# Performance work log

Measured on AMD Instinct MI355X. Metric: run time of the kernel, lower is better.

Reference implementation:

```python
import jax, jax.numpy as jnp
import numpy as np

D_MODEL = 1024
N_HEADS = 16
HEAD_DIM = D_MODEL // N_HEADS
D_FF = 4096
B, T = 2, 2048
LN_EPS = 1e-5


def setup_inputs() -> dict:
    key = jax.random.key(0)
    ks = jax.random.split(key, 12)
    s = 0.02
    return {
        "x": jax.random.normal(ks[0], (B, T, D_MODEL), jnp.float32),
        "ln1_g": jnp.ones((D_MODEL,), jnp.float32),
        "ln1_b": jnp.zeros((D_MODEL,), jnp.float32),
        "w_qkv": jax.random.normal(ks[1], (D_MODEL, 3 * D_MODEL), jnp.float32) * s,
        "b_qkv": jnp.zeros((3 * D_MODEL,), jnp.float32),
        "w_out": jax.random.normal(ks[2], (D_MODEL, D_MODEL), jnp.float32) * s,
        "b_out": jnp.zeros((D_MODEL,), jnp.float32),
        "ln2_g": jnp.ones((D_MODEL,), jnp.float32),
        "ln2_b": jnp.zeros((D_MODEL,), jnp.float32),
        "w_ff1": jax.random.normal(ks[3], (D_MODEL, D_FF), jnp.float32) * s,
        "b_ff1": jnp.zeros((D_FF,), jnp.float32),
        "w_ff2": jax.random.normal(ks[4], (D_FF, D_MODEL), jnp.float32) * s,
        "b_ff2": jnp.zeros((D_MODEL,), jnp.float32),
    }


def _layernorm(x, g, b):
    mu = jnp.mean(x, axis=-1, keepdims=True)
    var = jnp.mean(jnp.square(x - mu), axis=-1, keepdims=True)
    return (x - mu) * jax.lax.rsqrt(var + LN_EPS) * g + b


def _attention(h, w_qkv, b_qkv, w_out, b_out):
    Bx, Tx, C = h.shape
    qkv = h @ w_qkv + b_qkv  # [B,T,3C]
    q, k, v = jnp.split(qkv, 3, axis=-1)
    # [B,H,T,Dh]
    q = q.reshape(Bx, Tx, N_HEADS, HEAD_DIM).transpose(0, 2, 1, 3)
    k = k.reshape(Bx, Tx, N_HEADS, HEAD_DIM).transpose(0, 2, 1, 3)
    v = v.reshape(Bx, Tx, N_HEADS, HEAD_DIM).transpose(0, 2, 1, 3)
    scale = 1.0 / np.sqrt(HEAD_DIM).astype(np.float32)
    scores = jnp.einsum("bhqd,bhkd->bhqk", q, k) * scale
    causal = jnp.tril(jnp.ones((Tx, Tx), bool))
    scores = jnp.where(causal[None, None], scores, -jnp.inf)
    attn = jax.nn.softmax(scores, axis=-1)
    out = jnp.einsum("bhqk,bhkd->bhqd", attn, v)
    out = out.transpose(0, 2, 1, 3).reshape(Bx, Tx, C)
    return out @ w_out + b_out


def reference(x, ln1_g, ln1_b, w_qkv, b_qkv, w_out, b_out,
              ln2_g, ln2_b, w_ff1, b_ff1, w_ff2, b_ff2):
    h = _layernorm(x, ln1_g, ln1_b)
    x = x + _attention(h, w_qkv, b_qkv, w_out, b_out)
    h2 = _layernorm(x, ln2_g, ln2_b)
    ff = jax.nn.relu(h2 @ w_ff1 + b_ff1) @ w_ff2 + b_ff2
    return x + ff
```

## Files before the change

### kernel.cpp

```cpp
#include <hip/hip_runtime.h>


typedef unsigned short u16;
typedef __attribute__((ext_vector_type(8))) short     bf16x8;
typedef __attribute__((ext_vector_type(4))) float     f32x4;
typedef __attribute__((ext_vector_type(8))) unsigned short u16x8;
typedef __attribute__((ext_vector_type(4))) unsigned short u16x4;

__device__ __forceinline__ u16 f2bf(float f) {
    unsigned u = __builtin_bit_cast(unsigned, f);
    unsigned r = (u + 0x7fffu + ((u >> 16) & 1u)) >> 16;
    return (u16)r;
}
__device__ __forceinline__ float bf2f(u16 h) {
    unsigned u = ((unsigned)h) << 16;
    return __builtin_bit_cast(float, u);
}
__device__ __forceinline__ f32x4 mfma16(bf16x8 a, bf16x8 b, f32x4 c) {
    return __builtin_amdgcn_mfma_f32_16x16x32_bf16(a, b, c, 0, 0, 0);
}
__device__ __forceinline__ void gl_lds16(const u16* g, u16* l) {
    __builtin_amdgcn_global_load_lds((const __attribute__((address_space(1))) void*)g,
                                     (__attribute__((address_space(3))) void*)l, 16, 0, 0);
}

__global__ __launch_bounds__(256) void wconv_kernel(const float* __restrict__ in, u16* __restrict__ out,
                                                    int R, int C) {
    __shared__ float t[32][33];
    const int tx = threadIdx.x, ty = threadIdx.y;
    const int c0 = blockIdx.x * 32, r0 = blockIdx.y * 32;
#pragma unroll
    for (int i = 0; i < 4; ++i)
        t[ty + 8 * i][tx] = in[(size_t)(r0 + ty + 8 * i) * C + c0 + tx];
    __syncthreads();
#pragma unroll
    for (int i = 0; i < 4; ++i)
        out[(size_t)(c0 + ty + 8 * i) * R + r0 + tx] = f2bf(t[tx][ty + 8 * i]);
}

__global__ __launch_bounds__(256) void ln_kernel(const float* __restrict__ x, const float* __restrict__ g,
                                                 const float* __restrict__ b, u16* __restrict__ out) {
    const int row = blockIdx.x, tid = threadIdx.x;
    const float4 v = ((const float4*)(x + (size_t)row * 1024))[tid];
    float s = v.x + v.y + v.z + v.w;
    float q = v.x * v.x + v.y * v.y + v.z * v.z + v.w * v.w;
#pragma unroll
    for (int o = 32; o; o >>= 1) { s += __shfl_xor(s, o); q += __shfl_xor(q, o); }
    __shared__ float red[8];
    if ((tid & 63) == 0) { red[(tid >> 6) * 2] = s; red[(tid >> 6) * 2 + 1] = q; }
    __syncthreads();
    s = red[0] + red[2] + red[4] + red[6];
    q = red[1] + red[3] + red[5] + red[7];
    const float mu = s * (1.0f / 1024.0f);
    const float var = q * (1.0f / 1024.0f) - mu * mu;
    const float rs = rsqrtf(var + 1e-5f);
    const float4 gv = ((const float4*)g)[tid];
    const float4 bv = ((const float4*)b)[tid];
    u16x4 o;
    o[0] = f2bf((v.x - mu) * rs * gv.x + bv.x);
    o[1] = f2bf((v.y - mu) * rs * gv.y + bv.y);
    o[2] = f2bf((v.z - mu) * rs * gv.z + bv.z);
    o[3] = f2bf((v.w - mu) * rs * gv.w + bv.w);
    ((u16x4*)(out + (size_t)row * 1024))[tid] = o;
}

template <int MODE, int BN>
__global__ __launch_bounds__(256) void gemm_kernel(const u16* __restrict__ A, const u16* __restrict__ Bt,
                                                   const float* __restrict__ bias, const float* __restrict__ resid,
                                                   void* __restrict__ Cout, int M, int N, int K) {
    __shared__ __align__(16) u16 lds[2][2][4096];
    constexpr int MR = (BN == 128) ? 4 : 2;
    const int tid = threadIdx.x, lane = tid & 63, wid = tid >> 6;
    const int wr = (BN == 128) ? (wid >> 1) : wid;
    const int wc = (BN == 128) ? (wid & 1) : 0;
    const int lg = lane >> 4, lc = lane & 15;
    const int m0 = blockIdx.x * 128, n0 = blockIdx.y * BN;

    const u16* ga0 = A + (size_t)(m0 + (tid >> 2)) * K + (tid & 3) * 8;
    const u16* gb0 = Bt + (size_t)(n0 + (tid >> 2)) * K + (tid & 3) * 8;

    f32x4 acc[MR][4];
#pragma unroll
    for (int m = 0; m < MR; ++m)
#pragma unroll
        for (int n = 0; n < 4; ++n) acc[m][n] = (f32x4){0.f, 0.f, 0.f, 0.f};

    const int NT = K >> 5;
    auto stage = [&](int buf, int kt) {
        const u16* ga = ga0 + kt * 32;
        const u16* gb = gb0 + kt * 32;
        gl_lds16(ga, &lds[buf][0][tid * 8]);
        gl_lds16(ga + (size_t)64 * K, &lds[buf][0][2048 + tid * 8]);
        gl_lds16(gb, &lds[buf][1][tid * 8]);
        if (BN == 128) gl_lds16(gb + (size_t)64 * K, &lds[buf][1][2048 + tid * 8]);
    };
    stage(0, 0);
    for (int kt = 0; kt < NT; ++kt) {
        __syncthreads();
        if (kt + 1 < NT) stage((kt + 1) & 1, kt + 1);
        const u16* la = &lds[kt & 1][0][0];
        const u16* lb = &lds[kt & 1][1][0];
        bf16x8 a[MR], bb[4];
#pragma unroll
        for (int m = 0; m < MR; ++m) a[m] = *(const bf16x8*)(la + (wr * (MR * 16) + m * 16 + lc) * 32 + lg * 8);
#pragma unroll
        for (int n = 0; n < 4; ++n) bb[n] = *(const bf16x8*)(lb + (wc * 64 + n * 16 + lc) * 32 + lg * 8);
#pragma unroll
        for (int m = 0; m < MR; ++m)
#pragma unroll
            for (int n = 0; n < 4; ++n) acc[m][n] = mfma16(a[m], bb[n], acc[m][n]);
    }
#pragma unroll
    for (int m = 0; m < MR; ++m) {
        const int row = m0 + wr * (MR * 16) + m * 16 + lg * 4;
#pragma unroll
        for (int n = 0; n < 4; ++n) {
            const int col = n0 + wc * 64 + n * 16 + lc;
            const float bv = bias[col];
#pragma unroll
            for (int r = 0; r < 4; ++r) {
                float v = acc[m][n][r] + bv;
                if (MODE == 1) v = fmaxf(v, 0.0f);
                if (MODE == 2) {
                    v += resid[(size_t)(row + r) * N + col];
                    ((float*)Cout)[(size_t)(row + r) * N + col] = v;
                } else {
                    ((u16*)Cout)[(size_t)(row + r) * N + col] = f2bf(v);
                }
            }
        }
    }
}

__global__ __launch_bounds__(256) void vtrans_kernel(const u16* __restrict__ qkv, u16* __restrict__ v_t) {
    __shared__ u16 tile[64][72];
    const int bh = blockIdx.x >> 5, tt = blockIdx.x & 31;
    const int b = bh >> 4, h = bh & 15, t0 = tt * 64;
    const int tid = threadIdx.x;
    {
        const int tl = tid >> 2, seg = (tid & 3) * 16;
        const u16* src = qkv + (size_t)(b * 2048 + t0 + tl) * 3072 + 2048 + h * 64 + seg;
        u16x8 a = *(const u16x8*)src;
        u16x8 c = *(const u16x8*)(src + 8);
#pragma unroll
        for (int j = 0; j < 8; ++j) { tile[tl][seg + j] = a[j]; tile[tl][seg + 8 + j] = c[j]; }
    }
    __syncthreads();
    {
        const int d = tid >> 2, ts = (tid & 3) * 16;
        u16x8 o0, o1;
#pragma unroll
        for (int j = 0; j < 8; ++j) { o0[j] = tile[ts + j][d]; o1[j] = tile[ts + 8 + j][d]; }
        u16* dst = v_t + ((size_t)bh * 64 + d) * 2048 + t0 + ts;
        *(u16x8*)dst = o0;
        *(u16x8*)(dst + 8) = o1;
    }
}

__global__ __launch_bounds__(256) void attn_kernel(const u16* __restrict__ qkv, const u16* __restrict__ v_t,
                                                   u16* __restrict__ attnb) {
    __shared__ __align__(16) u16 wbuf[4][64 * 72];
    __shared__ float ml[4][2][64];
    const int tid = threadIdx.x, lane = tid & 63, wid = tid >> 6;
    const int lg = lane >> 4, lc = lane & 15;
    const int swz = (blockIdx.x & 7) * 64 + (blockIdx.x >> 3);
    const int j = swz & 15, bh = swz >> 4;
    const int b = bh >> 4, h = bh & 15;
    u16* pl = &wbuf[wid][0];

    const u16* qbase = qkv + (size_t)b * 2048 * 3072 + h * 64;
    const u16* kbase = qbase + 1024;

    for (int ph = 0; ph < 2; ++ph) {
        const int qt = ph ? (31 - j) : j;
        const int q0 = qt * 64;

        bf16x8 qf[2][4];
#pragma unroll
        for (int ks = 0; ks < 2; ++ks)
#pragma unroll
            for (int nf = 0; nf < 4; ++nf)
                qf[ks][nf] = *(const bf16x8*)(qbase + (size_t)(q0 + nf * 16 + lc) * 3072 + ks * 32 + lg * 8);

        f32x4 o[4][4];
#pragma unroll
        for (int i = 0; i < 4; ++i)
#pragma unroll
            for (int jj = 0; jj < 4; ++jj) o[i][jj] = (f32x4){0.f, 0.f, 0.f, 0.f};
        float mrow[4] = {-1e30f, -1e30f, -1e30f, -1e30f};
        float lrow[4] = {0.f, 0.f, 0.f, 0.f};

        const int nkt = 2 * qt + 2;
        for (int kt = wid; kt < nkt; kt += 4) {
            const int t0 = kt * 32;
            f32x4 s[2][4];
#pragma unroll
            for (int mf = 0; mf < 2; ++mf)
#pragma unroll
                for (int nf = 0; nf < 4; ++nf) s[mf][nf] = (f32x4){0.f, 0.f, 0.f, 0.f};
#pragma unroll
            for (int mf = 0; mf < 2; ++mf) {
                bf16x8 k0 = *(const bf16x8*)(kbase + (size_t)(t0 + mf * 16 + lc) * 3072 + lg * 8);
                bf16x8 k1 = *(const bf16x8*)(kbase + (size_t)(t0 + mf * 16 + lc) * 3072 + 32 + lg * 8);
#pragma unroll
                for (int nf = 0; nf < 4; ++nf) {
                    s[mf][nf] = mfma16(k0, qf[0][nf], s[mf][nf]);
                    s[mf][nf] = mfma16(k1, qf[1][nf], s[mf][nf]);
                }
            }
            const bool diag = (kt >= 2 * qt);
#pragma unroll
            for (int mf = 0; mf < 2; ++mf)
#pragma unroll
                for (int nf = 0; nf < 4; ++nf)
#pragma unroll
                    for (int r = 0; r < 4; ++r) {
                        float v = s[mf][nf][r] * 0.125f;
                        if (diag) {
                            const int kv = t0 + mf * 16 + lg * 4 + r;
                            const int qq = q0 + nf * 16 + lc;
                            if (kv > qq) v = -1e30f;
                        }
                        s[mf][nf][r] = v;
                    }
#pragma unroll
            for (int nf = 0; nf < 4; ++nf) {
                float cm = s[0][nf][0];
#pragma unroll
                for (int mf = 0; mf < 2; ++mf)
#pragma unroll
                    for (int r = 0; r < 4; ++r) cm = fmaxf(cm, s[mf][nf][r]);
                cm = fmaxf(cm, __shfl_xor(cm, 16));
                cm = fmaxf(cm, __shfl_xor(cm, 32));
                const float mn = fmaxf(mrow[nf], cm);
                const float fac = __expf(mrow[nf] - mn);
                mrow[nf] = mn;
                float cs = 0.f;
#pragma unroll
                for (int mf = 0; mf < 2; ++mf)
#pragma unroll
                    for (int r = 0; r < 4; ++r) {
                        const float p = __expf(s[mf][nf][r] - mn);
                        s[mf][nf][r] = p;
                        cs += p;
                    }
                cs += __shfl_xor(cs, 16);
                cs += __shfl_xor(cs, 32);
                lrow[nf] = lrow[nf] * fac + cs;
#pragma unroll
                for (int mf2 = 0; mf2 < 4; ++mf2) o[mf2][nf] *= fac;
#pragma unroll
                for (int mf = 0; mf < 2; ++mf) {
                    u16x4 pk;
                    pk[0] = f2bf(s[mf][nf][0]);
                    pk[1] = f2bf(s[mf][nf][1]);
                    pk[2] = f2bf(s[mf][nf][2]);
                    pk[3] = f2bf(s[mf][nf][3]);
                    *(u16x4*)(pl + (nf * 16 + lc) * 40 + mf * 16 + lg * 4) = pk;
                }
            }
            bf16x8 pb[4];
#pragma unroll
            for (int nf = 0; nf < 4; ++nf)
                pb[nf] = *(const bf16x8*)(pl + (nf * 16 + lc) * 40 + lg * 8);
#pragma unroll
            for (int mf2 = 0; mf2 < 4; ++mf2) {
                bf16x8 vf = *(const bf16x8*)(v_t + ((size_t)bh * 64 + mf2 * 16 + lc) * 2048 + t0 + lg * 8);
#pragma unroll
                for (int nf = 0; nf < 4; ++nf) o[mf2][nf] = mfma16(vf, pb[nf], o[mf2][nf]);
            }
        }
        u16* po = &wbuf[wid][0];
#pragma unroll
        for (int mf2 = 0; mf2 < 4; ++mf2)
#pragma unroll
            for (int nf = 0; nf < 4; ++nf) {
                u16x4 pk;
                pk[0] = f2bf(o[mf2][nf][0]);
                pk[1] = f2bf(o[mf2][nf][1]);
                pk[2] = f2bf(o[mf2][nf][2]);
                pk[3] = f2bf(o[mf2][nf][3]);
                *(u16x4*)(po + (nf * 16 + lc) * 72 + mf2 * 16 + lg * 4) = pk;
            }
        if (lg == 0) {
#pragma unroll
            for (int nf = 0; nf < 4; ++nf) {
                ml[wid][0][nf * 16 + lc] = mrow[nf];
                ml[wid][1][nf * 16 + lc] = lrow[nf];
            }
        }
        __syncthreads();
#pragma unroll
        for (int rep = 0; rep < 2; ++rep) {
            const int it = tid + rep * 256;
            const int q = it >> 3, oc = it & 7;
            float mv[4], lv[4];
#pragma unroll
            for (int w = 0; w < 4; ++w) { mv[w] = ml[w][0][q]; lv[w] = ml[w][1][q]; }
            const float M = fmaxf(fmaxf(mv[0], mv[1]), fmaxf(mv[2], mv[3]));
            float fw[4], L = 0.f;
#pragma unroll
            for (int w = 0; w < 4; ++w) { fw[w] = __expf(mv[w] - M); L += lv[w] * fw[w]; }
            const float invL = 1.0f / L;
            float acc[8] = {0.f, 0.f, 0.f, 0.f, 0.f, 0.f, 0.f, 0.f};
#pragma unroll
            for (int w = 0; w < 4; ++w) {
                u16x8 v = *(const u16x8*)(&wbuf[w][q * 72 + oc * 8]);
#pragma unroll
                for (int jj = 0; jj < 8; ++jj) acc[jj] += bf2f(v[jj]) * fw[w];
            }
            u16x8 ov;
#pragma unroll
            for (int jj = 0; jj < 8; ++jj) ov[jj] = f2bf(acc[jj] * invL);
            *(u16x8*)(attnb + (size_t)(b * 2048 + q0 + q) * 1024 + h * 64 + oc * 8) = ov;
        }
        __syncthreads();
    }
}

extern "C" void kernel_launch(void* const* d_in, const int* in_sizes, int n_in,
                              void* d_out, int out_size, void* d_ws, size_t ws_size,
                              hipStream_t stream) {
    const float* x = (const float*)d_in[0];
    const float* ln1_g = (const float*)d_in[1];
    const float* ln1_b = (const float*)d_in[2];
    const float* w_qkv = (const float*)d_in[3];
    const float* b_qkv = (const float*)d_in[4];
    const float* w_out = (const float*)d_in[5];
    const float* b_out = (const float*)d_in[6];
    const float* ln2_g = (const float*)d_in[7];
    const float* ln2_b = (const float*)d_in[8];
    const float* w_ff1 = (const float*)d_in[9];
    const float* b_ff1 = (const float*)d_in[10];
    const float* w_ff2 = (const float*)d_in[11];
    const float* b_ff2 = (const float*)d_in[12];
    float* out = (float*)d_out;
    char* ws = (char*)d_ws;

    u16* wTqkv = (u16*)(ws + 0);
    u16* wTout = (u16*)(ws + 6291456);
    u16* wTff1 = (u16*)(ws + 8388608);
    u16* wTff2 = (u16*)(ws + 16777216);
    u16* h1    = (u16*)(ws + 25165824);
    u16* qkv   = (u16*)(ws + 33554432);
    u16* v_t   = (u16*)(ws + 58720256);
    u16* attnb = (u16*)(ws + 67108864);
    float* x2  = (float*)(ws + 75497472);
    u16* h2    = (u16*)(ws + 92274688);
    u16* ff1   = (u16*)(ws + 25165824);

    wconv_kernel<<<dim3(96, 32), dim3(32, 8), 0, stream>>>(w_qkv, wTqkv, 1024, 3072);
    wconv_kernel<<<dim3(32, 32), dim3(32, 8), 0, stream>>>(w_out, wTout, 1024, 1024);
    wconv_kernel<<<dim3(128, 32), dim3(32, 8), 0, stream>>>(w_ff1, wTff1, 1024, 4096);
    wconv_kernel<<<dim3(32, 128), dim3(32, 8), 0, stream>>>(w_ff2, wTff2, 4096, 1024);

    ln_kernel<<<4096, 256, 0, stream>>>(x, ln1_g, ln1_b, h1);
    gemm_kernel<0, 128><<<dim3(32, 24), 256, 0, stream>>>(h1, wTqkv, b_qkv, nullptr, qkv, 4096, 3072, 1024);
    vtrans_kernel<<<1024, 256, 0, stream>>>(qkv, v_t);
    attn_kernel<<<512, 256, 0, stream>>>(qkv, v_t, attnb);
    gemm_kernel<2, 64><<<dim3(32, 16), 256, 0, stream>>>(attnb, wTout, b_out, x, x2, 4096, 1024, 1024);
    ln_kernel<<<4096, 256, 0, stream>>>(x2, ln2_g, ln2_b, h2);
    gemm_kernel<1, 128><<<dim3(32, 32), 256, 0, stream>>>(h2, wTff1, b_ff1, nullptr, ff1, 4096, 4096, 1024);
    gemm_kernel<2, 64><<<dim3(32, 16), 256, 0, stream>>>(ff1, wTff2, b_ff2, x2, out, 4096, 1024, 4096);
}
```

Measured before the change: 382.7 us.

## Use persistent attention with atomic work queue and 32-row query tiles

Attention becomes a persistent kernel. Blocks pull 32-row query tiles from an atomic counter, largest causal tiles first, replacing the fixed pairing of 64-row tiles. The exponentials switch to exp2 with the log2e factor folded into the scale, and bf16 packing uses the hardware v_cvt_pk_bf16_f32 instruction. This targets load imbalance and tail effects from the causal mask, at the cost of a memset, an atomic per task, and less Q reuse per tile.

```diff
diff --git a/kernel.cpp b/kernel.cpp
--- a/kernel.cpp
+++ b/kernel.cpp
@@ -6,6 +6,7 @@
 typedef __attribute__((ext_vector_type(4))) float     f32x4;
 typedef __attribute__((ext_vector_type(8))) unsigned short u16x8;
 typedef __attribute__((ext_vector_type(4))) unsigned short u16x4;
+typedef __attribute__((ext_vector_type(4))) unsigned int   u32x4;
 
 __device__ __forceinline__ u16 f2bf(float f) {
     unsigned u = __builtin_bit_cast(unsigned, f);
@@ -15,6 +16,12 @@
 __device__ __forceinline__ float bf2f(u16 h) {
     unsigned u = ((unsigned)h) << 16;
     return __builtin_bit_cast(float, u);
+}
+__device__ __forceinline__ float ex2(float x) { return __builtin_amdgcn_exp2f(x); }
+__device__ __forceinline__ unsigned cvtpk(float lo, float hi) {
+    unsigned r;
+    asm("v_cvt_pk_bf16_f32 %0, %1, %2" : "=v"(r) : "v"(lo), "v"(hi));
+    return r;
 }
 __device__ __forceinline__ f32x4 mfma16(bf16x8 a, bf16x8 b, f32x4 c) {
     return __builtin_amdgcn_mfma_f32_16x16x32_bf16(a, b, c, 0, 0, 0);
@@ -158,64 +165,68 @@
 }
 
 __global__ __launch_bounds__(256) void attn_kernel(const u16* __restrict__ qkv, const u16* __restrict__ v_t,
-                                                   u16* __restrict__ attnb) {
-    __shared__ __align__(16) u16 wbuf[4][64 * 72];
-    __shared__ float ml[4][2][64];
+                                                   u16* __restrict__ attnb, unsigned* __restrict__ qcnt) {
+    __shared__ __align__(16) u16 wbuf[4][32 * 72];
+    __shared__ float ml[4][2][32];
+    __shared__ int task_s;
     const int tid = threadIdx.x, lane = tid & 63, wid = tid >> 6;
     const int lg = lane >> 4, lc = lane & 15;
-    const int swz = (blockIdx.x & 7) * 64 + (blockIdx.x >> 3);
-    const int j = swz & 15, bh = swz >> 4;
-    const int b = bh >> 4, h = bh & 15;
     u16* pl = &wbuf[wid][0];
-
-    const u16* qbase = qkv + (size_t)b * 2048 * 3072 + h * 64;
-    const u16* kbase = qbase + 1024;
-
-    for (int ph = 0; ph < 2; ++ph) {
-        const int qt = ph ? (31 - j) : j;
-        const int q0 = qt * 64;
-
-        bf16x8 qf[2][4];
+    const float SC = 0.125f * 1.44269504f;
+
+    while (true) {
+        if (tid == 0) task_s = (int)atomicAdd(qcnt, 1u);
+        __syncthreads();
+        const int t = task_s;
+        if (t >= 2048) break;
+        const int qz = 63 - (t >> 5), bh = t & 31;
+        const int b = bh >> 4, h = bh & 15;
+        const int q0 = qz * 32;
+
+        const u16* qbase = qkv + (size_t)b * 2048 * 3072 + h * 64;
+        const u16* kbase = qbase + 1024;
+
+        bf16x8 qf[2][2];
 #pragma unroll
         for (int ks = 0; ks < 2; ++ks)
 #pragma unroll
-            for (int nf = 0; nf < 4; ++nf)
+            for (int nf = 0; nf < 2; ++nf)
                 qf[ks][nf] = *(const bf16x8*)(qbase + (size_t)(q0 + nf * 16 + lc) * 3072 + ks * 32 + lg * 8);
 
-        f32x4 o[4][4];
+        f32x4 o[4][2];
 #pragma unroll
         for (int i = 0; i < 4; ++i)
 #pragma unroll
-            for (int jj = 0; jj < 4; ++jj) o[i][jj] = (f32x4){0.f, 0.f, 0.f, 0.f};
-        float mrow[4] = {-1e30f, -1e30f, -1e30f, -1e30f};
-        float lrow[4] = {0.f, 0.f, 0.f, 0.f};
-
-        const int nkt = 2 * qt + 2;
+            for (int jj = 0; jj < 2; ++jj) o[i][jj] = (f32x4){0.f, 0.f, 0.f, 0.f};
+        float mrow[2] = {-1e30f, -1e30f};
+        float lrow[2] = {0.f, 0.f};
+
+        const int nkt = qz + 1;
         for (int kt = wid; kt < nkt; kt += 4) {
             const int t0 = kt * 32;
-            f32x4 s[2][4];
+            f32x4 s[2][2];
 #pragma unroll
             for (int mf = 0; mf < 2; ++mf)
 #pragma unroll
-                for (int nf = 0; nf < 4; ++nf) s[mf][nf] = (f32x4){0.f, 0.f, 0.f, 0.f};
+                for (int nf = 0; nf < 2; ++nf) s[mf][nf] = (f32x4){0.f, 0.f, 0.f, 0.f};
 #pragma unroll
             for (int mf = 0; mf < 2; ++mf) {
                 bf16x8 k0 = *(const bf16x8*)(kbase + (size_t)(t0 + mf * 16 + lc) * 3072 + lg * 8);
                 bf16x8 k1 = *(const bf16x8*)(kbase + (size_t)(t0 + mf * 16 + lc) * 3072 + 32 + lg * 8);
 #pragma unroll
-                for (int nf = 0; nf < 4; ++nf) {
+                for (int nf = 0; nf < 2; ++nf) {
                     s[mf][nf] = mfma16(k0, qf[0][nf], s[mf][nf]);
                     s[mf][nf] = mfma16(k1, qf[1][nf], s[mf][nf]);
                 }
             }
-            const bool diag = (kt >= 2 * qt);
+            const bool diag = (kt == qz);
 #pragma unroll
             for (int mf = 0; mf < 2; ++mf)
 #pragma unroll
-                for (int nf = 0; nf < 4; ++nf)
+                for (int nf = 0; nf < 2; ++nf)
 #pragma unroll
                     for (int r = 0; r < 4; ++r) {
-                        float v = s[mf][nf][r] * 0.125f;
+                        float v = s[mf][nf][r] * SC;
                         if (diag) {
                             const int kv = t0 + mf * 16 + lg * 4 + r;
                             const int qq = q0 + nf * 16 + lc;
@@ -224,7 +235,7 @@
                         s[mf][nf][r] = v;
                     }
 #pragma unroll
-            for (int nf = 0; nf < 4; ++nf) {
+            for (int nf = 0; nf < 2; ++nf) {
                 float cm = s[0][nf][0];
 #pragma unroll
                 for (int mf = 0; mf < 2; ++mf)
@@ -233,14 +244,14 @@
                 cm = fmaxf(cm, __shfl_xor(cm, 16));
                 cm = fmaxf(cm, __shfl_xor(cm, 32));
                 const float mn = fmaxf(mrow[nf], cm);
-                const float fac = __expf(mrow[nf] - mn);
+                const float fac = ex2(mrow[nf] - mn);
                 mrow[nf] = mn;
                 float cs = 0.f;
 #pragma unroll
                 for (int mf = 0; mf < 2; ++mf)
 #pragma unroll
                     for (int r = 0; r < 4; ++r) {
-                        const float p = __expf(s[mf][nf][r] - mn);
+                        const float p = ex2(s[mf][nf][r] - mn);
                         s[mf][nf][r] = p;
                         cs += p;
                     }
@@ -251,56 +262,50 @@
                 for (int mf2 = 0; mf2 < 4; ++mf2) o[mf2][nf] *= fac;
 #pragma unroll
                 for (int mf = 0; mf < 2; ++mf) {
-                    u16x4 pk;
-                    pk[0] = f2bf(s[mf][nf][0]);
-                    pk[1] = f2bf(s[mf][nf][1]);
-                    pk[2] = f2bf(s[mf][nf][2]);
-                    pk[3] = f2bf(s[mf][nf][3]);
-                    *(u16x4*)(pl + (nf * 16 + lc) * 40 + mf * 16 + lg * 4) = pk;
+                    uint2 pk;
+                    pk.x = cvtpk(s[mf][nf][0], s[mf][nf][1]);
+                    pk.y = cvtpk(s[mf][nf][2], s[mf][nf][3]);
+                    *(uint2*)(pl + (nf * 16 + lc) * 40 + mf * 16 + lg * 4) = pk;
                 }
             }
-            bf16x8 pb[4];
-#pragma unroll
-            for (int nf = 0; nf < 4; ++nf)
+            bf16x8 pb[2];
+#pragma unroll
+            for (int nf = 0; nf < 2; ++nf)
                 pb[nf] = *(const bf16x8*)(pl + (nf * 16 + lc) * 40 + lg * 8);
 #pragma unroll
             for (int mf2 = 0; mf2 < 4; ++mf2) {
                 bf16x8 vf = *(const bf16x8*)(v_t + ((size_t)bh * 64 + mf2 * 16 + lc) * 2048 + t0 + lg * 8);
 #pragma unroll
-                for (int nf = 0; nf < 4; ++nf) o[mf2][nf] = mfma16(vf, pb[nf], o[mf2][nf]);
+                for (int nf = 0; nf < 2; ++nf) o[mf2][nf] = mfma16(vf, pb[nf], o[mf2][nf]);
             }
         }
         u16* po = &wbuf[wid][0];
 #pragma unroll
         for (int mf2 = 0; mf2 < 4; ++mf2)
 #pragma unroll
-            for (int nf = 0; nf < 4; ++nf) {
-                u16x4 pk;
-                pk[0] = f2bf(o[mf2][nf][0]);
-                pk[1] = f2bf(o[mf2][nf][1]);
-                pk[2] = f2bf(o[mf2][nf][2]);
-                pk[3] = f2bf(o[mf2][nf][3]);
-                *(u16x4*)(po + (nf * 16 + lc) * 72 + mf2 * 16 + lg * 4) = pk;
+            for (int nf = 0; nf < 2; ++nf) {
+                uint2 pk;
+                pk.x = cvtpk(o[mf2][nf][0], o[mf2][nf][1]);
+                pk.y = cvtpk(o[mf2][nf][2], o[mf2][nf][3]);
+                *(uint2*)(po + (nf * 16 + lc) * 72 + mf2 * 16 + lg * 4) = pk;
             }
         if (lg == 0) {
 #pragma unroll
-            for (int nf = 0; nf < 4; ++nf) {
+            for (int nf = 0; nf < 2; ++nf) {
                 ml[wid][0][nf * 16 + lc] = mrow[nf];
                 ml[wid][1][nf * 16 + lc] = lrow[nf];
             }
         }
         __syncthreads();
-#pragma unroll
-        for (int rep = 0; rep < 2; ++rep) {
-            const int it = tid + rep * 256;
-            const int q = it >> 3, oc = it & 7;
+        {
+            const int q = tid >> 3, oc = tid & 7;
             float mv[4], lv[4];
 #pragma unroll
             for (int w = 0; w < 4; ++w) { mv[w] = ml[w][0][q]; lv[w] = ml[w][1][q]; }
             const float M = fmaxf(fmaxf(mv[0], mv[1]), fmaxf(mv[2], mv[3]));
             float fw[4], L = 0.f;
 #pragma unroll
-            for (int w = 0; w < 4; ++w) { fw[w] = __expf(mv[w] - M); L += lv[w] * fw[w]; }
+            for (int w = 0; w < 4; ++w) { fw[w] = ex2(mv[w] - M); L += lv[w] * fw[w]; }
             const float invL = 1.0f / L;
             float acc[8] = {0.f, 0.f, 0.f, 0.f, 0.f, 0.f, 0.f, 0.f};
 #pragma unroll
@@ -309,10 +314,10 @@
 #pragma unroll
                 for (int jj = 0; jj < 8; ++jj) acc[jj] += bf2f(v[jj]) * fw[w];
             }
-            u16x8 ov;
-#pragma unroll
-            for (int jj = 0; jj < 8; ++jj) ov[jj] = f2bf(acc[jj] * invL);
-            *(u16x8*)(attnb + (size_t)(b * 2048 + q0 + q) * 1024 + h * 64 + oc * 8) = ov;
+            u32x4 ov;
+#pragma unroll
+            for (int jj = 0; jj < 4; ++jj) ov[jj] = cvtpk(acc[2 * jj] * invL, acc[2 * jj + 1] * invL);
+            *(u32x4*)(attnb + (size_t)(b * 2048 + q0 + q) * 1024 + h * 64 + oc * 8) = ov;
         }
         __syncthreads();
     }
@@ -348,6 +353,7 @@
     float* x2  = (float*)(ws + 75497472);
     u16* h2    = (u16*)(ws + 92274688);
     u16* ff1   = (u16*)(ws + 25165824);
+    unsigned* qcnt = (unsigned*)(ws + 75497472);
 
     wconv_kernel<<<dim3(96, 32), dim3(32, 8), 0, stream>>>(w_qkv, wTqkv, 1024, 3072);
     wconv_kernel<<<dim3(32, 32), dim3(32, 8), 0, stream>>>(w_out, wTout, 1024, 1024);
@@ -357,7 +363,8 @@
     ln_kernel<<<4096, 256, 0, stream>>>(x, ln1_g, ln1_b, h1);
     gemm_kernel<0, 128><<<dim3(32, 24), 256, 0, stream>>>(h1, wTqkv, b_qkv, nullptr, qkv, 4096, 3072, 1024);
     vtrans_kernel<<<1024, 256, 0, stream>>>(qkv, v_t);
-    attn_kernel<<<512, 256, 0, stream>>>(qkv, v_t, attnb);
+    (void)hipMemsetAsync(qcnt, 0, 4, stream);
+    attn_kernel<<<1024, 256, 0, stream>>>(qkv, v_t, attnb, qcnt);
     gemm_kernel<2, 64><<<dim3(32, 16), 256, 0, stream>>>(attnb, wTout, b_out, x, x2, 4096, 1024, 1024);
     ln_kernel<<<4096, 256, 0, stream>>>(x2, ln2_g, ln2_b, h2);
     gemm_kernel<1, 128><<<dim3(32, 32), 256, 0, stream>>>(h2, wTff1, b_ff1, nullptr, ff1, 4096, 4096, 1024);
```

New measurement: 389.7 us. About the same (+1.8%).
